# Performance work log

Hardware: AMD Instinct MI355X
Metric: run time of the kernel (lower is better)

## Reference

```python
import jax, jax.numpy as jnp
import numpy as np

N = 50000      # nodes
E = 800000     # edges
D = 128        # in_channels
H = 128        # hidden_channels
G = 64         # graphs in batch
OUT = 10       # out_channels
L = 6          # gcn layers (hardcoded in module)
EPS = 1e-5     # batchnorm eps


def setup_inputs() -> dict:
    key = jax.random.key(0)
    ks = jax.random.split(key, 8)
    s = 1.0 / np.sqrt(H)
    return {
        "x": jax.random.normal(ks[0], (N, D), jnp.float32),
        "edge_index": jax.random.randint(ks[1], (2, E), 0, N),
        "batch": jnp.sort(jax.random.randint(ks[2], (N,), 0, G)),
        "conv_W": jax.random.normal(ks[3], (L, D, H), jnp.float32) * s,
        "conv_b": jnp.zeros((L, H), jnp.float32),
        "bn_gamma": jnp.ones((L - 1, H), jnp.float32),
        "bn_beta": jnp.zeros((L - 1, H), jnp.float32),
        "head_W1": jax.random.normal(ks[4], (H, H), jnp.float32) * s,
        "head_b1": jnp.zeros((H,), jnp.float32),
        "head_bn_gamma": jnp.ones((H,), jnp.float32),
        "head_bn_beta": jnp.zeros((H,), jnp.float32),
        "head_W2": jax.random.normal(ks[5], (H, H), jnp.float32) * s,
        "head_b2": jnp.zeros((H,), jnp.float32),
        "head_W3": jax.random.normal(ks[6], (H, OUT), jnp.float32) * s,
        "head_b3": jnp.zeros((OUT,), jnp.float32),
    }


def _batchnorm(h, gamma, beta):
    # track_running_stats=False -> always batch statistics, biased variance
    mu = h.mean(axis=0)
    var = jnp.mean((h - mu) ** 2, axis=0)
    return (h - mu) * jax.lax.rsqrt(var + EPS) * gamma + beta


def reference(x, edge_index, batch, conv_W, conv_b, bn_gamma, bn_beta,
              head_W1, head_b1, head_bn_gamma, head_bn_beta,
              head_W2, head_b2, head_W3, head_b3):
    src, dst = edge_index[0], edge_index[1]
    # GCN symmetric norm with self-loops: deg = in-degree + 1
    deg = jnp.zeros((N,), x.dtype).at[dst].add(1.0) + 1.0
    dinv = jax.lax.rsqrt(deg)                 # deg^{-1/2}
    enorm = (dinv[src] * dinv[dst])[:, None]  # [E,1] edge weights
    self_w = (dinv * dinv)[:, None]           # [N,1] self-loop weight = 1/deg

    h = x
    for i in range(L):
        h = h @ conv_W[i]                                     # [N,H]
        agg = jnp.zeros_like(h).at[dst].add(h[src] * enorm)   # scatter-add
        h = agg + h * self_w + conv_b[i]
        if i < L - 1:
            h = jax.nn.relu(_batchnorm(h, bn_gamma[i], bn_beta[i]))
            # dropout(p=0.1) -> identity in eval

    # global_mean_pool over graphs
    counts = jnp.zeros((G,), h.dtype).at[batch].add(1.0)
    pooled = jnp.zeros((G, H), h.dtype).at[batch].add(h)
    pooled = pooled / jnp.clip(counts, 1.0)[:, None]

    # prediction head: Linear -> BN -> ReLU -> (Dropout) -> Linear -> ReLU -> Linear
    z = pooled @ head_W1 + head_b1
    z = jax.nn.relu(_batchnorm(z, head_bn_gamma, head_bn_beta))
    z = jax.nn.relu(z @ head_W2 + head_b2)
    return z @ head_W3 + head_b3
```

## Files before the change

### kernel.cpp

```cpp
#include <hip/hip_runtime.h>

#define N 50000
#define E 800000
#define H 128
#define G 64
#define OUTC 10
#define L 6
#define EPS 1e-5f
#define SLOTS 64

typedef unsigned short ushort_t;
typedef __attribute__((ext_vector_type(8))) short short8;
typedef __attribute__((ext_vector_type(8))) unsigned short ushort8;
typedef __attribute__((ext_vector_type(4))) float floatx4;

__device__ __forceinline__ void atomAddF(float* p, float v) {
  unsafeAtomicAdd(p, v);
}

__device__ __forceinline__ unsigned short f2bf(float f) {
  unsigned u = __float_as_uint(f);
  unsigned r = (u + 0x7FFF + ((u >> 16) & 1)) >> 16;
  return (unsigned short)r;
}
__device__ __forceinline__ float bf2f(unsigned short b) {
  return __uint_as_float(((unsigned)b) << 16);
}

__global__ void zero_kernel(int* __restrict__ p, int n) {
  int i = blockIdx.x * blockDim.x + threadIdx.x;
  if (i < n) p[i] = 0;
}

__global__ void csr_fill_kernel(const int* __restrict__ src, const int* __restrict__ dst,
                                int* __restrict__ cnt, ushort_t* __restrict__ csru) {
  int e = blockIdx.x * blockDim.x + threadIdx.x;
  if (e < E) {
    int d = dst[e];
    int pos = atomicAdd(&cnt[d], 1);
    if (pos < SLOTS) csru[(d << 6) + pos] = (ushort_t)src[e];
  }
}

__global__ void dinv_kernel(const int* __restrict__ cnt, float* __restrict__ dinv) {
  int n = blockIdx.x * blockDim.x + threadIdx.x;
  if (n < N) dinv[n] = rsqrtf((float)(cnt[n] + 1));
}

__global__ void prep_kernel(const float* __restrict__ convW, ushort_t* __restrict__ WT) {
  int j = blockIdx.x * 256 + threadIdx.x;
  if (j < L * H * H) {
    int l = j >> 14, r = j & 16383;
    int n = r >> 7, k = r & 127;
    WT[j] = f2bf(convW[l * 16384 + k * 128 + n]);
  }
}

__global__ void cnt_kernel(const int* __restrict__ batch, float* __restrict__ cntg) {
  __shared__ int lb[G + 1];
  int t = threadIdx.x;
  if (t <= G) {
    int lo = 0, hi = N;
    while (lo < hi) { int m = (lo + hi) >> 1; if (batch[m] < t) lo = m + 1; else hi = m; }
    lb[t] = lo;
  }
  __syncthreads();
  if (t < G) cntg[t] = (float)(lb[t + 1] - lb[t]);
}

__global__ __launch_bounds__(256) void gemm_mfma_kernel(
    const ushort_t* __restrict__ Ab, const float* __restrict__ Af,
    const ushort_t* __restrict__ WT,
    const float* __restrict__ dinv, ushort_t* __restrict__ hWs,
    const float* __restrict__ bnsums, const float* __restrict__ gamma,
    const float* __restrict__ beta)
{
  const int tid = threadIdx.x;
  const int wave = tid >> 6, lane = tid & 63;
  const int quad = lane >> 4, m = lane & 15;
  const int row0 = blockIdx.x * 64 + wave * 16;
  const int arow = min(row0 + m, N - 1);
  const float invN = 1.0f / (float)N;

  short8 afrag[4];
  if (Af) {
#pragma unroll
    for (int kc = 0; kc < 4; ++kc) {
      const float* p = &Af[arow * H + kc * 32 + quad * 8];
      float4 f0 = *(const float4*)p;
      float4 f1 = *(const float4*)(p + 4);
      short8 a;
      a[0] = (short)f2bf(f0.x); a[1] = (short)f2bf(f0.y);
      a[2] = (short)f2bf(f0.z); a[3] = (short)f2bf(f0.w);
      a[4] = (short)f2bf(f1.x); a[5] = (short)f2bf(f1.y);
      a[6] = (short)f2bf(f1.z); a[7] = (short)f2bf(f1.w);
      afrag[kc] = a;
    }
  } else {
#pragma unroll
    for (int kc = 0; kc < 4; ++kc) {
      ushort8 raw = *(const ushort8*)&Ab[arow * H + kc * 32 + quad * 8];
      if (bnsums) {
        const int k0 = kc * 32 + quad * 8;
#pragma unroll
        for (int j = 0; j < 8; ++j) {
          float s = bnsums[k0 + j], q = bnsums[128 + k0 + j];
          float mu = s * invN;
          float var = q * invN - mu * mu;
          float rs = rsqrtf(var + EPS);
          float sc = gamma[k0 + j] * rs;
          float sh = beta[k0 + j] - mu * sc;
          raw[j] = f2bf(fmaxf(bf2f(raw[j]) * sc + sh, 0.f));
        }
      }
      short8 a;
#pragma unroll
      for (int j = 0; j < 8; ++j) a[j] = (short)raw[j];
      afrag[kc] = a;
    }
  }

  float dv[4];
#pragma unroll
  for (int i = 0; i < 4; ++i) {
    int r = row0 + quad * 4 + i;
    dv[i] = (r < N) ? dinv[r] : 0.f;
  }

  const short* WTs = (const short*)WT;
#pragma unroll
  for (int nt = 0; nt < 8; ++nt) {
    floatx4 acc = {0.f, 0.f, 0.f, 0.f};
#pragma unroll
    for (int kc = 0; kc < 4; ++kc) {
      short8 bfrag = *(const short8*)&WTs[(nt * 16 + m) * H + kc * 32 + quad * 8];
      acc = __builtin_amdgcn_mfma_f32_16x16x32_bf16(afrag[kc], bfrag, acc, 0, 0, 0);
    }
    int col = nt * 16 + m;
#pragma unroll
    for (int i = 0; i < 4; ++i) {
      int r = row0 + quad * 4 + i;
      if (r < N) hWs[r * H + col] = f2bf(acc[i] * dv[i]);
    }
  }
}

__global__ __launch_bounds__(256) void gather_kernel(
    const ushort_t* __restrict__ hWs, const ushort_t* __restrict__ csru,
    const int* __restrict__ cnt, const float* __restrict__ dinv,
    const float* __restrict__ bias, ushort_t* __restrict__ aggb)
{
  int t = blockIdx.x * 256 + threadIdx.x;
  int n = t >> 4, c8 = (t & 15) * 8;

  ushort8 us = *(const ushort8*)&hWs[n * H + c8];
  float acc[8];
#pragma unroll
  for (int j = 0; j < 8; ++j) acc[j] = bf2f(us[j]);

  const int base = n << 6;
  const int deg = min(cnt[n], SLOTS);
  int e = 0;
  for (; e + 8 <= deg; e += 8) {
    ushort8 idx = *(const ushort8*)&csru[base + e];
    ushort8 u0 = *(const ushort8*)&hWs[(int)idx[0] * H + c8];
    ushort8 u1 = *(const ushort8*)&hWs[(int)idx[1] * H + c8];
    ushort8 u2 = *(const ushort8*)&hWs[(int)idx[2] * H + c8];
    ushort8 u3 = *(const ushort8*)&hWs[(int)idx[3] * H + c8];
    ushort8 u4 = *(const ushort8*)&hWs[(int)idx[4] * H + c8];
    ushort8 u5 = *(const ushort8*)&hWs[(int)idx[5] * H + c8];
    ushort8 u6 = *(const ushort8*)&hWs[(int)idx[6] * H + c8];
    ushort8 u7 = *(const ushort8*)&hWs[(int)idx[7] * H + c8];
#pragma unroll
    for (int j = 0; j < 8; ++j)
      acc[j] += ((bf2f(u0[j]) + bf2f(u1[j])) + (bf2f(u2[j]) + bf2f(u3[j]))) +
                ((bf2f(u4[j]) + bf2f(u5[j])) + (bf2f(u6[j]) + bf2f(u7[j])));
  }
  for (; e < deg; ++e) {
    int s0 = csru[base + e];
    ushort8 u0 = *(const ushort8*)&hWs[s0 * H + c8];
#pragma unroll
    for (int j = 0; j < 8; ++j) acc[j] += bf2f(u0[j]);
  }

  float dn = dinv[n];
  float4 b0 = *(const float4*)&bias[c8];
  float4 b1 = *(const float4*)&bias[c8 + 4];
  float bb[8] = {b0.x, b0.y, b0.z, b0.w, b1.x, b1.y, b1.z, b1.w};
  ushort8 o;
#pragma unroll
  for (int j = 0; j < 8; ++j) o[j] = f2bf(acc[j] * dn + bb[j]);
  *(ushort8*)&aggb[n * H + c8] = o;
}

__global__ __launch_bounds__(256) void bn_stats_kernel(
    const ushort_t* __restrict__ a, float* __restrict__ sums)
{
  __shared__ float redS[4 * 128], redQ[4 * 128];
  int tid = threadIdx.x;
  int cg = tid & 15, nn = tid >> 4;
  int c8 = cg * 8;
  int r0 = blockIdx.x * 128;
  float s[8], q[8];
#pragma unroll
  for (int j = 0; j < 8; ++j) { s[j] = 0.f; q[j] = 0.f; }
#pragma unroll
  for (int i = 0; i < 8; ++i) {
    int r = r0 + i * 16 + nn;
    if (r < N) {
      ushort8 u = *(const ushort8*)&a[r * H + c8];
#pragma unroll
      for (int j = 0; j < 8; ++j) { float v = bf2f(u[j]); s[j] += v; q[j] += v * v; }
    }
  }
  int wave = tid >> 6, lane = tid & 63;
#pragma unroll
  for (int j = 0; j < 8; ++j) {
    s[j] += __shfl_xor(s[j], 16); s[j] += __shfl_xor(s[j], 32);
    q[j] += __shfl_xor(q[j], 16); q[j] += __shfl_xor(q[j], 32);
  }
  if (lane < 16) {
#pragma unroll
    for (int j = 0; j < 8; ++j) {
      redS[wave * 128 + lane * 8 + j] = s[j];
      redQ[wave * 128 + lane * 8 + j] = q[j];
    }
  }
  __syncthreads();
  if (tid < 128) {
    float v = redS[tid] + redS[128 + tid] + redS[256 + tid] + redS[384 + tid];
    atomAddF(&sums[tid], v);
  } else {
    int t2 = tid - 128;
    float v = redQ[t2] + redQ[128 + t2] + redQ[256 + t2] + redQ[384 + t2];
    atomAddF(&sums[128 + t2], v);
  }
}

__global__ __launch_bounds__(256) void pool_kernel(
    const ushort_t* __restrict__ h, const int* __restrict__ batch,
    float* __restrict__ pooled )
{
  int r0 = blockIdx.x * 128;
  int rend = min(r0 + 128, N);
  int c = threadIdx.x & 127, half = threadIdx.x >> 7;
  float acc = 0.f;
  int curg = -1;
  for (int r = r0 + half; r < rend; r += 2) {
    int g = batch[r];
    if (g != curg) {
      if (curg >= 0) atomAddF(&pooled[curg * H + c], acc);
      acc = 0.f; curg = g;
    }
    acc += bf2f(h[r * H + c]);
  }
  if (curg >= 0) atomAddF(&pooled[curg * H + c], acc);
}

__global__ void head1_kernel(const float* __restrict__ pooled, const float* __restrict__ cntg,
                             const float* __restrict__ W1, const float* __restrict__ b1,
                             float* __restrict__ z1)
{
  int t = blockIdx.x * 256 + threadIdx.x;
  int g = t >> 7, c = t & 127;
  float s = 0.f;
  for (int k = 0; k < H; ++k) s += pooled[g * H + k] * W1[k * H + c];
  z1[t] = s / fmaxf(cntg[g], 1.0f) + b1[c];
}

__global__ void head_bn_kernel(float* __restrict__ z1,
                               const float* __restrict__ gamma, const float* __restrict__ beta)
{
  int c = threadIdx.x;
  float s = 0.f, q = 0.f;
  for (int g = 0; g < G; ++g) { float v = z1[g * H + c]; s += v; q += v * v; }
  float mu = s / (float)G;
  float var = q / (float)G - mu * mu;
  float rs = rsqrtf(var + EPS);
  float ga = gamma[c], be = beta[c];
  for (int g = 0; g < G; ++g) {
    float v = z1[g * H + c];
    z1[g * H + c] = fmaxf((v - mu) * rs * ga + be, 0.f);
  }
}

__global__ void head2_kernel(const float* __restrict__ z1, const float* __restrict__ W2,
                             const float* __restrict__ b2, float* __restrict__ z2)
{
  int t = blockIdx.x * 256 + threadIdx.x;
  int g = t >> 7, c = t & 127;
  float s = b2[c];
  for (int k = 0; k < H; ++k) s += z1[g * H + k] * W2[k * H + c];
  z2[t] = fmaxf(s, 0.f);
}

__global__ void head3_kernel(const float* __restrict__ z2, const float* __restrict__ W3,
                             const float* __restrict__ b3, float* __restrict__ out)
{
  int t = blockIdx.x * 256 + threadIdx.x;
  if (t < G * OUTC) {
    int g = t / OUTC, o = t % OUTC;
    float s = b3[o];
    for (int k = 0; k < H; ++k) s += z2[g * H + k] * W3[k * OUTC + o];
    out[t] = s;
  }
}

extern "C" void kernel_launch(void* const* d_in, const int* in_sizes, int n_in,
                              void* d_out, int out_size, void* d_ws, size_t ws_size,
                              hipStream_t stream) {
  const float* x     = (const float*)d_in[0];
  const int*   ei    = (const int*)d_in[1];
  const int*   srcp  = ei;
  const int*   dstp  = ei + E;
  const int*   batch = (const int*)d_in[2];
  const float* convW = (const float*)d_in[3];
  const float* convb = (const float*)d_in[4];
  const float* bng   = (const float*)d_in[5];
  const float* bnb   = (const float*)d_in[6];
  const float* W1    = (const float*)d_in[7];
  const float* b1    = (const float*)d_in[8];
  const float* hg    = (const float*)d_in[9];
  const float* hb    = (const float*)d_in[10];
  const float* W2    = (const float*)d_in[11];
  const float* b2    = (const float*)d_in[12];
  const float* W3    = (const float*)d_in[13];
  const float* b3    = (const float*)d_in[14];
  float* out = (float*)d_out;

  const size_t NH2 = (size_t)N * H / 2;
  float*    ws     = (float*)d_ws;
  ushort_t* aggb   = (ushort_t*)ws;
  ushort_t* hWs    = (ushort_t*)(ws + NH2);
  ushort_t* WT     = (ushort_t*)(ws + 2 * NH2);
  float*    dinv   = ws + 2 * NH2 + (L * H * H / 2);
  ushort_t* csru   = (ushort_t*)(dinv + N);
  int*      cnt    = (int*)(csru + (size_t)N * SLOTS);
  float*    bnsums = (float*)(cnt + N);
  float*    pooled = bnsums + (L - 1) * 256;
  float*    cntg   = pooled + G * H;
  float*    z1     = cntg + G;
  float*    z2     = z1 + G * H;

  const int zero_words = N + (L - 1) * 256 + G * H;
  zero_kernel<<<(zero_words + 255) / 256, 256, 0, stream>>>(cnt, zero_words);
  csr_fill_kernel<<<(E + 255) / 256, 256, 0, stream>>>(srcp, dstp, cnt, csru);
  dinv_kernel<<<(N + 255) / 256, 256, 0, stream>>>(cnt, dinv);
  cnt_kernel<<<1, 128, 0, stream>>>(batch, cntg);
  prep_kernel<<<(L * H * H + 255) / 256, 256, 0, stream>>>(convW, WT);

  for (int l = 0; l < L; ++l) {
    const ushort_t* Ab = (l == 0) ? nullptr : aggb;
    const float*    Af = (l == 0) ? x : nullptr;
    const float* bs = (l == 0) ? nullptr : bnsums + (l - 1) * 256;
    const float* ga = (l == 0) ? nullptr : bng + (size_t)(l - 1) * H;
    const float* be = (l == 0) ? nullptr : bnb + (size_t)(l - 1) * H;
    gemm_mfma_kernel<<<(N + 63) / 64, 256, 0, stream>>>(
        Ab, Af, WT + (size_t)l * H * H, dinv, hWs, bs, ga, be);
    gather_kernel<<<N * 16 / 256, 256, 0, stream>>>(
        hWs, csru, cnt, dinv, convb + (size_t)l * H, aggb);
    if (l < L - 1)
      bn_stats_kernel<<<(N + 127) / 128, 256, 0, stream>>>(aggb, bnsums + l * 256);
  }

  pool_kernel<<<(N + 127) / 128, 256, 0, stream>>>(aggb, batch, pooled);
  head1_kernel<<<32, 256, 0, stream>>>(pooled, cntg, W1, b1, z1);
  head_bn_kernel<<<1, 128, 0, stream>>>(z1, hg, hb);
  head2_kernel<<<32, 256, 0, stream>>>(z1, W2, b2, z2);
  head3_kernel<<<3, 256, 0, stream>>>(z2, W3, b3, out);
}
```

Before: 618.2 us.

## Fuse batchnorm statistics into gather kernel with per-block partials

Computes the per-channel sum and sum of squares for batchnorm inside the gather kernel, from the fp32 outputs before bf16 rounding. Each block writes a partial row to a workspace buffer, and a small reduction kernel then accumulates these rows atomically into the stats. This removes the separate pass that reread the whole bf16 aggregate in every layer, at the cost of an extra syncthreads in the gather kernel and a second small launch. Statistics now come from unrounded values, which changes numerics slightly.

```diff
diff --git a/kernel.cpp b/kernel.cpp
--- a/kernel.cpp
+++ b/kernel.cpp
@@ -8,6 +8,7 @@
 #define L 6
 #define EPS 1e-5f
 #define SLOTS 64
+#define GA_BLOCKS (N * 16 / 256)
 
 typedef unsigned short ushort_t;
 typedef __attribute__((ext_vector_type(8))) short short8;
@@ -148,9 +149,12 @@
 __global__ __launch_bounds__(256) void gather_kernel(
     const ushort_t* __restrict__ hWs, const ushort_t* __restrict__ csru,
     const int* __restrict__ cnt, const float* __restrict__ dinv,
-    const float* __restrict__ bias, ushort_t* __restrict__ aggb)
-{
-  int t = blockIdx.x * 256 + threadIdx.x;
+    const float* __restrict__ bias, ushort_t* __restrict__ aggb,
+    float* __restrict__ partials)
+{
+  __shared__ float redS[4 * 128], redQ[4 * 128];
+  int tid = threadIdx.x;
+  int t = blockIdx.x * 256 + tid;
   int n = t >> 4, c8 = (t & 15) * 8;
 
   ushort8 us = *(const ushort8*)&hWs[n * H + c8];
@@ -187,54 +191,52 @@
   float4 b0 = *(const float4*)&bias[c8];
   float4 b1 = *(const float4*)&bias[c8 + 4];
   float bb[8] = {b0.x, b0.y, b0.z, b0.w, b1.x, b1.y, b1.z, b1.w};
+  float of[8];
   ushort8 o;
 #pragma unroll
-  for (int j = 0; j < 8; ++j) o[j] = f2bf(acc[j] * dn + bb[j]);
+  for (int j = 0; j < 8; ++j) {
+    of[j] = acc[j] * dn + bb[j];
+    o[j] = f2bf(of[j]);
+  }
   *(ushort8*)&aggb[n * H + c8] = o;
-}
-
-__global__ __launch_bounds__(256) void bn_stats_kernel(
-    const ushort_t* __restrict__ a, float* __restrict__ sums)
-{
-  __shared__ float redS[4 * 128], redQ[4 * 128];
+
+  if (partials) {
+    int wave = tid >> 6, lane = tid & 63;
+    float s[8], q[8];
+#pragma unroll
+    for (int j = 0; j < 8; ++j) { s[j] = of[j]; q[j] = of[j] * of[j]; }
+#pragma unroll
+    for (int j = 0; j < 8; ++j) {
+      s[j] += __shfl_xor(s[j], 16); s[j] += __shfl_xor(s[j], 32);
+      q[j] += __shfl_xor(q[j], 16); q[j] += __shfl_xor(q[j], 32);
+    }
+    if (lane < 16) {
+#pragma unroll
+      for (int j = 0; j < 8; ++j) {
+        redS[wave * 128 + lane * 8 + j] = s[j];
+        redQ[wave * 128 + lane * 8 + j] = q[j];
+      }
+    }
+    __syncthreads();
+    float* prow = &partials[(size_t)blockIdx.x * 256];
+    if (tid < 128) {
+      prow[tid] = redS[tid] + redS[128 + tid] + redS[256 + tid] + redS[384 + tid];
+    } else {
+      int t2 = tid - 128;
+      prow[tid] = redQ[t2] + redQ[128 + t2] + redQ[256 + t2] + redQ[384 + t2];
+    }
+  }
+}
+
+__global__ __launch_bounds__(256) void bn_reduce_kernel(
+    const float* __restrict__ partials, float* __restrict__ sums)
+{
   int tid = threadIdx.x;
-  int cg = tid & 15, nn = tid >> 4;
-  int c8 = cg * 8;
-  int r0 = blockIdx.x * 128;
-  float s[8], q[8];
-#pragma unroll
-  for (int j = 0; j < 8; ++j) { s[j] = 0.f; q[j] = 0.f; }
-#pragma unroll
-  for (int i = 0; i < 8; ++i) {
-    int r = r0 + i * 16 + nn;
-    if (r < N) {
-      ushort8 u = *(const ushort8*)&a[r * H + c8];
-#pragma unroll
-      for (int j = 0; j < 8; ++j) { float v = bf2f(u[j]); s[j] += v; q[j] += v * v; }
-    }
-  }
-  int wave = tid >> 6, lane = tid & 63;
-#pragma unroll
-  for (int j = 0; j < 8; ++j) {
-    s[j] += __shfl_xor(s[j], 16); s[j] += __shfl_xor(s[j], 32);
-    q[j] += __shfl_xor(q[j], 16); q[j] += __shfl_xor(q[j], 32);
-  }
-  if (lane < 16) {
-#pragma unroll
-    for (int j = 0; j < 8; ++j) {
-      redS[wave * 128 + lane * 8 + j] = s[j];
-      redQ[wave * 128 + lane * 8 + j] = q[j];
-    }
-  }
-  __syncthreads();
-  if (tid < 128) {
-    float v = redS[tid] + redS[128 + tid] + redS[256 + tid] + redS[384 + tid];
-    atomAddF(&sums[tid], v);
-  } else {
-    int t2 = tid - 128;
-    float v = redQ[t2] + redQ[128 + t2] + redQ[256 + t2] + redQ[384 + t2];
-    atomAddF(&sums[128 + t2], v);
-  }
+  int r0 = blockIdx.x * 49;
+  int r1 = min(r0 + 49, GA_BLOCKS);
+  float v = 0.f;
+  for (int r = r0; r < r1; ++r) v += partials[(size_t)r * 256 + tid];
+  atomAddF(&sums[tid], v);
 }
 
 __global__ __launch_bounds__(256) void pool_kernel(
@@ -341,6 +343,7 @@
   float*    cntg   = pooled + G * H;
   float*    z1     = cntg + G;
   float*    z2     = z1 + G * H;
+  float*    partials = z2 + G * H;
 
   const int zero_words = N + (L - 1) * 256 + G * H;
   zero_kernel<<<(zero_words + 255) / 256, 256, 0, stream>>>(cnt, zero_words);
@@ -357,10 +360,11 @@
     const float* be = (l == 0) ? nullptr : bnb + (size_t)(l - 1) * H;
     gemm_mfma_kernel<<<(N + 63) / 64, 256, 0, stream>>>(
         Ab, Af, WT + (size_t)l * H * H, dinv, hWs, bs, ga, be);
-    gather_kernel<<<N * 16 / 256, 256, 0, stream>>>(
-        hWs, csru, cnt, dinv, convb + (size_t)l * H, aggb);
+    float* part = (l < L - 1) ? partials : nullptr;
+    gather_kernel<<<GA_BLOCKS, 256, 0, stream>>>(
+        hWs, csru, cnt, dinv, convb + (size_t)l * H, aggb, part);
     if (l < L - 1)
-      bn_stats_kernel<<<(N + 127) / 128, 256, 0, stream>>>(aggb, bnsums + l * 256);
+      bn_reduce_kernel<<<64, 256, 0, stream>>>(partials, bnsums + l * 256);
   }
 
   pool_kernel<<<(N + 127) / 128, 256, 0, stream>>>(aggb, batch, pooled);
```

Measured after the change: 642.5 us. +3.9%, slower.
